# Performance work log

Hardware: AMD Instinct MI355X
Metric: run time of the kernel (lower is better)

The kernel has to match this reference:

```python
import jax, jax.numpy as jnp
import numpy as np
import math

TOPK = 13
NUM_CLASSES = 80
ALPHA = 1.0
BETA = 6.0
EPS = 1e-9


def ciou_xyxy(box1, box2, eps=1e-7):
    """CIoU between xyxy boxes; box1/box2 broadcastable [..., 4]. Returns [..., 1]."""
    b1x1, b1y1, b1x2, b1y2 = jnp.split(box1, 4, axis=-1)
    b2x1, b2y1, b2x2, b2y2 = jnp.split(box2, 4, axis=-1)
    w1, h1 = b1x2 - b1x1, b1y2 - b1y1 + eps
    w2, h2 = b2x2 - b2x1, b2y2 - b2y1 + eps
    inter = (jnp.minimum(b1x2, b2x2) - jnp.maximum(b1x1, b2x1)).clip(0) * \
            (jnp.minimum(b1y2, b2y2) - jnp.maximum(b1y1, b2y1)).clip(0)
    union = w1 * h1 + w2 * h2 - inter + eps
    iou = inter / union
    cw = jnp.maximum(b1x2, b2x2) - jnp.minimum(b1x1, b2x1)
    ch = jnp.maximum(b1y2, b2y2) - jnp.minimum(b1y1, b2y1)
    c2 = cw ** 2 + ch ** 2 + eps
    rho2 = ((b2x1 + b2x2 - b1x1 - b1x2) ** 2 + (b2y1 + b2y2 - b1y1 - b1y2) ** 2) / 4
    v = (4.0 / math.pi ** 2) * (jnp.arctan(w2 / h2) - jnp.arctan(w1 / h1)) ** 2
    alpha = jax.lax.stop_gradient(v / (v - iou + (1 + eps)))  # torch.no_grad block
    return iou - (rho2 / c2 + v * alpha)


def setup_inputs() -> dict:
    key = jax.random.key(0)
    ks = jax.random.split(key, 8)
    bs, M = 16, 64
    # YOLOv8 anchor grid: strides 8/16/32 on a 640x640 image -> 8400 points
    pts = []
    for s, n in ((8, 80), (16, 40), (32, 20)):
        xs = (np.arange(n, dtype=np.float32) + 0.5) * s
        gx, gy = np.meshgrid(xs, xs)
        pts.append(np.stack([gx.ravel(), gy.ravel()], -1))
    anc_points = jnp.asarray(np.concatenate(pts, 0), jnp.float32)  # (8400, 2)
    A = anc_points.shape[0]
    pd_scores = jax.random.uniform(ks[0], (bs, A, NUM_CLASSES), jnp.float32)
    c = jax.random.uniform(ks[1], (bs, A, 2), jnp.float32) * 640.0
    wh = jax.random.uniform(ks[2], (bs, A, 2), jnp.float32) * 120.0 + 8.0
    pd_bboxes = jnp.concatenate([c - wh / 2, c + wh / 2], -1)  # xyxy
    gc = jax.random.uniform(ks[3], (bs, M, 2), jnp.float32) * 560.0 + 40.0
    gwh = jax.random.uniform(ks[4], (bs, M, 2), jnp.float32) * 200.0 + 20.0
    gt_bboxes = jnp.concatenate([gc - gwh / 2, gc + gwh / 2], -1)
    gt_labels = jax.random.randint(ks[5], (bs, M, 1), 0, NUM_CLASSES, dtype=jnp.int32)
    mask_gt = (jax.random.uniform(ks[6], (bs, M, 1)) > 0.25).astype(jnp.float32)
    return {"pd_scores": pd_scores, "pd_bboxes": pd_bboxes, "anc_points": anc_points,
            "gt_labels": gt_labels, "gt_bboxes": gt_bboxes, "mask_gt": mask_gt}


def _assign(pd_scores, pd_bboxes, anc_points, gt_labels, gt_bboxes, mask_gt):
    bs, A, nc = pd_scores.shape
    M = gt_bboxes.shape[1]
    dt = pd_scores.dtype

    # ---- select_candidates_in_gts: anchors inside gt boxes -> (b, M, A) ----
    lt = gt_bboxes[:, :, None, :2]            # (b, M, 1, 2)
    rb = gt_bboxes[:, :, None, 2:]
    xy = anc_points[None, None]               # (1, 1, A, 2)
    deltas = jnp.concatenate([xy - lt, rb - xy], axis=-1)  # (b, M, A, 4)
    mask_in_gts = (deltas.min(-1) > EPS).astype(dt)        # (b, M, A)

    # ---- get_box_metrics ----
    bidx = jnp.arange(bs)[:, None]                         # (b, 1)
    labels = gt_labels[..., 0].astype(jnp.int32)           # (b, M)
    bbox_scores = pd_scores[bidx, :, labels]               # (b, M, A)
    overlaps = ciou_xyxy(gt_bboxes[:, :, None, :], pd_bboxes[:, None, :, :])
    overlaps = overlaps[..., 0].clip(0)                    # (b, M, A)
    align_metric = bbox_scores ** ALPHA * overlaps ** BETA

    # ---- select_topk_candidates (scatter-add instead of one_hot over 8400) ----
    metrics = align_metric * mask_in_gts
    _, topk_idxs = jax.lax.top_k(metrics, TOPK)            # (b, M, topk)
    valid = mask_gt > 0                                    # (b, M, 1) bool
    topk_idxs = jnp.where(valid, topk_idxs, 0)
    counts = jnp.zeros((bs, M, A), dt).at[
        jnp.arange(bs)[:, None, None], jnp.arange(M)[None, :, None], topk_idxs
    ].add(1.0)
    mask_topk = jnp.where(counts > 1, jnp.zeros((), dt), counts)
    mask_pos = mask_topk * mask_in_gts * mask_gt           # (b, M, A)

    # ---- select_highest_overlaps (unconditional; identity when no conflicts) ----
    fg_mask = mask_pos.sum(-2)                             # (b, A)
    mask_multi = fg_mask[:, None, :] > 1                   # (b, 1, A)
    max_idx = overlaps.argmax(1)                           # (b, A)
    is_max = jnp.swapaxes(jax.nn.one_hot(max_idx, M, dtype=dt), 1, 2)  # (b, M, A)
    mask_pos = jnp.where(mask_multi, is_max, mask_pos)
    fg_mask = mask_pos.sum(-2)
    target_gt_idx = mask_pos.argmax(-2)                    # (b, A)

    # ---- get_targets ----
    flat_idx = target_gt_idx + bidx * M                    # (b, A) into b*M
    target_labels = jnp.clip(gt_labels.reshape(-1)[flat_idx], 0)   # (b, A)
    target_bboxes = gt_bboxes.reshape(-1, 4)[flat_idx]             # (b, A, 4)
    target_scores = jax.nn.one_hot(target_labels, NUM_CLASSES, dtype=dt)
    target_scores = jnp.where(fg_mask[..., None] > 0, target_scores, jnp.zeros((), dt))

    # ---- normalize scores by aligned metric ----
    align_metric = align_metric * mask_pos
    pos_align = align_metric.max(-1, keepdims=True)        # (b, M, 1)
    pos_overlaps = (overlaps * mask_pos).max(-1, keepdims=True)
    norm = (align_metric * pos_overlaps / (pos_align + EPS)).max(-2)[..., None]  # (b, A, 1)
    target_scores = target_scores * norm

    return target_labels, target_bboxes, target_scores, fg_mask.astype(bool), target_gt_idx


def reference(pd_scores, pd_bboxes, anc_points, gt_labels, gt_bboxes, mask_gt):
    return _assign(pd_scores, pd_bboxes, anc_points, gt_labels, gt_bboxes, mask_gt)
```

## Files before the change

kernel.cpp:

```cpp
#include <hip/hip_runtime.h>

#define A_TOT 8400
#define NCLS  80
#define MGT   64
#define TK    13
#define NT    256
#define EPS7  1e-7f
#define EPS9  1e-9f
#define INV_PI2 0.4052847345693511f

__device__ __forceinline__ float ciou_clip(
    float gx1, float gy1, float gx2, float gy2, float ga, float area1,
    float px1, float py1, float px2, float py2, float pa)
{
  float w2 = px2 - px1, h2 = py2 - py1 + EPS7;
  float iw = fmaxf(fminf(gx2, px2) - fmaxf(gx1, px1), 0.f);
  float ih = fmaxf(fminf(gy2, py2) - fmaxf(gy1, py1), 0.f);
  float inter = iw * ih;
  float uni = area1 + w2 * h2 - inter + EPS7;
  float iou = inter / uni;
  float cw = fmaxf(gx2, px2) - fminf(gx1, px1);
  float ch = fmaxf(gy2, py2) - fminf(gy1, py1);
  float c2 = cw * cw + ch * ch + EPS7;
  float dx = px1 + px2 - gx1 - gx2;
  float dy = py1 + py2 - gy1 - gy2;
  float rho2 = (dx * dx + dy * dy) * 0.25f;
  float dd = pa - ga;
  float v = INV_PI2 * dd * dd;
  float alpha = v / (v - iou + (1.f + EPS7));
  float c = iou - (rho2 / c2 + v * alpha);
  return fmaxf(c, 0.f);
}

__device__ __forceinline__ unsigned long long wmax64(unsigned long long k) {
#pragma unroll
  for (int s = 32; s > 0; s >>= 1) {
    unsigned long long o = __shfl_xor(k, s, 64);
    k = (o > k) ? o : k;
  }
  return k;
}

__global__ __launch_bounds__(NT)
void k_topk(const float* __restrict__ pd_scores,
            const float* __restrict__ pd_bboxes,
            const float* __restrict__ anc,
            const int* __restrict__ gt_labels,
            const float* __restrict__ gt_bboxes,
            const float* __restrict__ mask_gt,
            unsigned long long* __restrict__ mask64)
{
  int row = blockIdx.x;
  if (mask_gt[row] <= 0.f) return;
  int b = row >> 6;
  int m = row & 63;
  int tid = threadIdx.x, lane = tid & 63, wid = tid >> 6;

  float4 g = ((const float4*)gt_bboxes)[row];
  float ga = atanf((g.z - g.x) / (g.w - g.y + EPS7));
  float area1 = (g.z - g.x) * (g.w - g.y + EPS7);
  int label = gt_labels[row];
  const float*  ps   = pd_scores + (size_t)b * A_TOT * NCLS + label;
  const float4* pb   = (const float4*)(pd_bboxes + (size_t)b * A_TOT * 4);
  const float2* anc2 = (const float2*)anc;

  unsigned long long l[TK];
#pragma unroll
  for (int k = 0; k < TK; ++k) l[k] = 0ULL;

  auto insert = [&](unsigned long long key) {
    if (key > l[TK - 1]) {
#pragma unroll
      for (int j = TK - 1; j > 0; --j) {
        unsigned long long prev = l[j - 1];
        l[j] = (key > prev) ? prev : ((key > l[j]) ? key : l[j]);
      }
      l[0] = (key > l[0]) ? key : l[0];
    }
  };
  auto eval_inbox = [&](int a) -> unsigned long long {
    float4 p = pb[a];
    float pa = atanf((p.z - p.x) / (p.w - p.y + EPS7));
    float ov = ciou_clip(g.x, g.y, g.z, g.w, ga, area1, p.x, p.y, p.z, p.w, pa);
    float o2 = ov * ov;
    float metric = ps[(size_t)a * NCLS] * (o2 * o2 * o2);
    return (((unsigned long long)__float_as_uint(metric)) << 32) |
           (unsigned long long)(~(unsigned)a);
  };

  {
    int a = tid;
    float2 an = anc2[a];
    float dmin = fminf(fminf(an.x - g.x, an.y - g.y), fminf(g.z - an.x, g.w - an.y));
    unsigned long long key = (unsigned long long)(~(unsigned)a);
    if (dmin > EPS9) key = eval_inbox(a);
    insert(key);
  }

  const int   ns[3] = {80, 40, 20};
  const float ss[3] = {8.f, 16.f, 32.f};
  const int   bb[3] = {0, 6400, 8000};
#pragma unroll
  for (int sc = 0; sc < 3; ++sc) {
    int n = ns[sc]; float s = ss[sc]; int base = bb[sc];
    float inv_s = 1.f / s;
    int xlo = max(0,     (int)floorf(g.x * inv_s - 0.5f));
    int xhi = min(n - 1, (int)ceilf (g.z * inv_s - 0.5f));
    int ylo = max(0,     (int)floorf(g.y * inv_s - 0.5f));
    int yhi = min(n - 1, (int)ceilf (g.w * inv_s - 0.5f));
    int nx = xhi - xlo + 1, ny = yhi - ylo + 1;
    if (nx <= 0 || ny <= 0) continue;
    int tot = nx * ny;
    float invnx = 1.f / (float)nx;
    for (int r = tid; r < tot; r += NT) {
      int q  = (int)floorf(((float)r + 0.5f) * invnx);
      int ix = xlo + (r - q * nx);
      int iy = ylo + q;
      int a = base + iy * n + ix;
      if (a < NT) continue;
      float ax = ((float)ix + 0.5f) * s;
      float ay = ((float)iy + 0.5f) * s;
      float dmin = fminf(fminf(ax - g.x, ay - g.y), fminf(g.z - ax, g.w - ay));
      if (dmin > EPS9) insert(eval_inbox(a));
    }
  }

  __shared__ unsigned long long sk[4 * TK];
  unsigned long long wres = 0ULL;
#pragma unroll
  for (int r = 0; r < TK; ++r) {
    unsigned long long w = wmax64(l[0]);
    if (lane == r) wres = w;
    if (l[0] == w) {
#pragma unroll
      for (int j = 0; j < TK - 1; ++j) l[j] = l[j + 1];
      l[TK - 1] = 0ULL;
    }
  }
  if (lane < TK) sk[wid * TK + lane] = wres;
  __syncthreads();

  if (wid == 0) {
    unsigned long long c = (lane < 4 * TK) ? sk[lane] : 0ULL;
    unsigned long long res = 0ULL;
#pragma unroll
    for (int r = 0; r < TK; ++r) {
      unsigned long long w = wmax64(c);
      if (lane == r) res = w;
      if (c == w) c = 0ULL;
    }
    if (lane < TK) {
      unsigned a = ~(unsigned)res;
      float2 an = anc2[a];
      float dmin = fminf(fminf(an.x - g.x, an.y - g.y), fminf(g.z - an.x, g.w - an.y));
      if (dmin > EPS9)
        atomicOr(mask64 + (size_t)b * A_TOT + a, 1ULL << m);
    }
  }
}

__global__ __launch_bounds__(256)
void k_resolve(const float* __restrict__ pd_scores,
               const float* __restrict__ pd_bboxes,
               const int* __restrict__ gt_labels,
               const float* __restrict__ gt_bboxes,
               const unsigned long long* __restrict__ mask64,
               int* __restrict__ tgt_ws, float* __restrict__ am_ws,
               unsigned int* __restrict__ pos_al, unsigned int* __restrict__ pos_ov,
               int total)
{
  int t = blockIdx.x * 256 + threadIdx.x;
  bool valid = t < total;
  unsigned long long msk = valid ? mask64[t] : 0ULL;
  int pc = __popcll(msk);
  float4 p = make_float4(0.f, 0.f, 0.f, 0.f);
  float pa_own = 0.f;
  if (valid && pc >= 1) {
    p = ((const float4*)pd_bboxes)[t];
    pa_own = atanf((p.z - p.x) / (p.w - p.y + EPS7));
  }
  if (valid && pc == 0) tgt_ws[t] = -1;
  if (valid && pc == 1) {
    int b = t / A_TOT;
    int tgt = __ffsll(msk) - 1;
    int gi = b * MGT + tgt;
    float4 g = ((const float4*)gt_bboxes)[gi];
    float ga = atanf((g.z - g.x) / (g.w - g.y + EPS7));
    float area1 = (g.z - g.x) * (g.w - g.y + EPS7);
    float ov = ciou_clip(g.x, g.y, g.z, g.w, ga, area1,
                         p.x, p.y, p.z, p.w, pa_own);
    int label = gt_labels[gi];
    float sc = pd_scores[(size_t)t * NCLS + label];
    float o2 = ov * ov;
    float am = sc * (o2 * o2 * o2);
    tgt_ws[t] = tgt; am_ws[t] = am;
    atomicMax(pos_al + gi, __float_as_uint(am));
    atomicMax(pos_ov + gi, __float_as_uint(ov));
  }
  unsigned long long mb = __ballot(valid && pc > 1);
  int lane = threadIdx.x & 63;
  while (mb) {
    int src = __ffsll(mb) - 1; mb &= mb - 1;
    int   tt  = __shfl(t, src);
    float px1 = __shfl(p.x, src), py1 = __shfl(p.y, src);
    float px2 = __shfl(p.z, src), py2 = __shfl(p.w, src);
    float pa  = __shfl(pa_own, src);
    int bb2 = tt / A_TOT;
    int gi = bb2 * MGT + lane;
    float4 g = ((const float4*)gt_bboxes)[gi];
    float ga = atanf((g.z - g.x) / (g.w - g.y + EPS7));
    float area1 = (g.z - g.x) * (g.w - g.y + EPS7);
    float ov = ciou_clip(g.x, g.y, g.z, g.w, ga, area1,
                         px1, py1, px2, py2, pa);
    unsigned long long key =
        (((unsigned long long)__float_as_uint(ov)) << 6) | (unsigned)(63 - lane);
    unsigned long long w = wmax64(key);
    if (key == w) {
      int label = gt_labels[gi];
      float sc = pd_scores[(size_t)tt * NCLS + label];
      float o2 = ov * ov;
      float am = sc * (o2 * o2 * o2);
      tgt_ws[tt] = lane; am_ws[tt] = am;
      atomicMax(pos_al + gi, __float_as_uint(am));
      atomicMax(pos_ov + gi, __float_as_uint(ov));
    }
  }
}

__global__ __launch_bounds__(256)
void k_write(const int* __restrict__ tgt_ws, const float* __restrict__ am_ws,
             const unsigned int* __restrict__ pos_al,
             const unsigned int* __restrict__ pos_ov,
             const int* __restrict__ gt_labels, const float* __restrict__ gt_bboxes,
             float* __restrict__ out, int bs)
{
  __shared__ int   slab[256];
  __shared__ float snorm[256];
  int total = bs * A_TOT;
  int base = blockIdx.x * 256;
  int t = base + threadIdx.x;
  int nrows = total - base; if (nrows > 256) nrows = 256;
  size_t OFF_BOX = (size_t)total;
  size_t OFF_SCR = OFF_BOX + (size_t)total * 4;
  size_t OFF_FG  = OFF_SCR + (size_t)total * NCLS;
  size_t OFF_TGT = OFF_FG + (size_t)total;
  if (t < total) {
    int b = t / A_TOT;
    int tw = tgt_ws[t];
    bool fg = tw >= 0;
    int tgt = fg ? tw : 0;
    int gi = b * MGT + tgt;
    int lab = gt_labels[gi]; if (lab < 0) lab = 0;
    float4 box = ((const float4*)gt_bboxes)[gi];
    float nrm = 0.f;
    if (fg) {
      float pa_ = __uint_as_float(pos_al[gi]);
      float po  = __uint_as_float(pos_ov[gi]);
      nrm = am_ws[t] * po / (pa_ + EPS9);
    }
    out[t] = (float)lab;
    ((float4*)(out + OFF_BOX))[t] = box;
    out[OFF_FG + t]  = fg ? 1.f : 0.f;
    out[OFF_TGT + t] = (float)tgt;
    slab[threadIdx.x]  = lab;
    snorm[threadIdx.x] = nrm;
  }
  __syncthreads();
  float4* srow = (float4*)(out + OFF_SCR + (size_t)base * NCLS);
  int nvec = nrows * (NCLS / 4);
  for (int u = threadIdx.x; u < nvec; u += 256) {
    int i  = u / (NCLS / 4);
    int c0 = (u - i * (NCLS / 4)) * 4;
    int lb = slab[i]; float nv = snorm[i];
    float4 v;
    v.x = (lb == c0    ) ? nv : 0.f;
    v.y = (lb == c0 + 1) ? nv : 0.f;
    v.z = (lb == c0 + 2) ? nv : 0.f;
    v.w = (lb == c0 + 3) ? nv : 0.f;
    srow[u] = v;
  }
}

extern "C" void kernel_launch(void* const* d_in, const int* in_sizes, int n_in,
                              void* d_out, int out_size, void* d_ws, size_t ws_size,
                              hipStream_t stream)
{
  const float* pd_scores = (const float*)d_in[0];
  const float* pd_bboxes = (const float*)d_in[1];
  const float* anc       = (const float*)d_in[2];
  const int*   gt_labels = (const int*)d_in[3];
  const float* gt_bboxes = (const float*)d_in[4];
  const float* mask_gt   = (const float*)d_in[5];
  int bs = in_sizes[0] / (A_TOT * NCLS);
  int NA = bs * A_TOT, NM = bs * MGT;

  unsigned long long* mask64 = (unsigned long long*)d_ws;
  unsigned int* pos_al = (unsigned int*)(mask64 + NA);
  unsigned int* pos_ov = pos_al + NM;
  int*   tgt_ws = (int*)(pos_ov + NM);
  float* am_ws  = (float*)(tgt_ws + NA);

  hipMemsetAsync(mask64, 0, (size_t)NA * 8 + (size_t)NM * 8, stream);

  k_topk<<<NM, NT, 0, stream>>>(pd_scores, pd_bboxes, anc, gt_labels, gt_bboxes,
                                mask_gt, mask64);
  k_resolve<<<(NA + 255) / 256, 256, 0, stream>>>(pd_scores, pd_bboxes, gt_labels,
                                                  gt_bboxes, mask64,
                                                  tgt_ws, am_ws, pos_al, pos_ov, NA);
  k_write<<<(NA + 255) / 256, 256, 0, stream>>>(tgt_ws, am_ws, pos_al, pos_ov,
                                                gt_labels, gt_bboxes, (float*)d_out, bs);
}
```

Measured before the change: 128.7 us.

## Fuse memset, top-k, resolve and write into one cooperative persistent kernel

Replaces the workspace memset and the three separate kernel launches with one cooperative kernel. It zeroes the workspace itself and separates the phases with grid-wide syncs, looping over rows and tiles with grid-stride loops. The aim is to remove per-launch overhead and the gaps between dependent launches. In exchange it adds three grid barriers and caps the grid at the co-resident block count. It also hardcodes 256 CUs in the grid size and keeps the old multi-kernel path as a fallback if the cooperative launch fails.

```diff
diff --git a/kernel.cpp b/kernel.cpp
--- a/kernel.cpp
+++ b/kernel.cpp
@@ -1,10 +1,12 @@
 #include <hip/hip_runtime.h>
+#include <hip/hip_cooperative_groups.h>
+
+namespace cg = cooperative_groups;
 
 #define A_TOT 8400
 #define NCLS  80
 #define MGT   64
 #define TK    13
-#define NT    256
 #define EPS7  1e-7f
 #define EPS9  1e-9f
 #define INV_PI2 0.4052847345693511f
@@ -41,28 +43,29 @@
   return k;
 }
 
-__global__ __launch_bounds__(NT)
-void k_topk(const float* __restrict__ pd_scores,
-            const float* __restrict__ pd_bboxes,
-            const float* __restrict__ anc,
-            const int* __restrict__ gt_labels,
-            const float* __restrict__ gt_bboxes,
-            const float* __restrict__ mask_gt,
-            unsigned long long* __restrict__ mask64)
-{
-  int row = blockIdx.x;
+
+__device__ __forceinline__ void topk_row_body(
+    int row, int tid,
+    const float* __restrict__ pd_scores,
+    const float* __restrict__ pd_bboxes,
+    const float2* __restrict__ anc2,
+    const int* __restrict__ gt_labels,
+    const float4* __restrict__ gb,
+    const float* __restrict__ mask_gt,
+    unsigned long long* __restrict__ mask64,
+    unsigned long long* sk)
+{
   if (mask_gt[row] <= 0.f) return;
   int b = row >> 6;
   int m = row & 63;
-  int tid = threadIdx.x, lane = tid & 63, wid = tid >> 6;
-
-  float4 g = ((const float4*)gt_bboxes)[row];
+  int lane = tid & 63, wid = tid >> 6;
+
+  float4 g = gb[row];
   float ga = atanf((g.z - g.x) / (g.w - g.y + EPS7));
   float area1 = (g.z - g.x) * (g.w - g.y + EPS7);
   int label = gt_labels[row];
-  const float*  ps   = pd_scores + (size_t)b * A_TOT * NCLS + label;
-  const float4* pb   = (const float4*)(pd_bboxes + (size_t)b * A_TOT * 4);
-  const float2* anc2 = (const float2*)anc;
+  const float*  ps = pd_scores + (size_t)b * A_TOT * NCLS + label;
+  const float4* pb = (const float4*)(pd_bboxes + (size_t)b * A_TOT * 4);
 
   unsigned long long l[TK];
 #pragma unroll
@@ -112,12 +115,12 @@
     if (nx <= 0 || ny <= 0) continue;
     int tot = nx * ny;
     float invnx = 1.f / (float)nx;
-    for (int r = tid; r < tot; r += NT) {
+    for (int r = tid; r < tot; r += 256) {
       int q  = (int)floorf(((float)r + 0.5f) * invnx);
       int ix = xlo + (r - q * nx);
       int iy = ylo + q;
       int a = base + iy * n + ix;
-      if (a < NT) continue;
+      if (a < 256) continue;
       float ax = ((float)ix + 0.5f) * s;
       float ay = ((float)iy + 0.5f) * s;
       float dmin = fminf(fminf(ax - g.x, ay - g.y), fminf(g.z - ax, g.w - ay));
@@ -125,7 +128,6 @@
     }
   }
 
-  __shared__ unsigned long long sk[4 * TK];
   unsigned long long wres = 0ULL;
 #pragma unroll
   for (int r = 0; r < TK; ++r) {
@@ -159,18 +161,17 @@
   }
 }
 
-__global__ __launch_bounds__(256)
-void k_resolve(const float* __restrict__ pd_scores,
-               const float* __restrict__ pd_bboxes,
-               const int* __restrict__ gt_labels,
-               const float* __restrict__ gt_bboxes,
-               const unsigned long long* __restrict__ mask64,
-               int* __restrict__ tgt_ws, float* __restrict__ am_ws,
-               unsigned int* __restrict__ pos_al, unsigned int* __restrict__ pos_ov,
-               int total)
-{
-  int t = blockIdx.x * 256 + threadIdx.x;
-  bool valid = t < total;
+__device__ __forceinline__ void resolve_body(
+    int t, bool valid,
+    const float* __restrict__ pd_scores,
+    const float* __restrict__ pd_bboxes,
+    const int* __restrict__ gt_labels,
+    const float4* __restrict__ gb,
+    const unsigned long long* __restrict__ mask64,
+    int* __restrict__ tgt_ws, float* __restrict__ am_ws,
+    unsigned int* __restrict__ pos_al, unsigned int* __restrict__ pos_ov)
+{
+  int lane = threadIdx.x & 63;
   unsigned long long msk = valid ? mask64[t] : 0ULL;
   int pc = __popcll(msk);
   float4 p = make_float4(0.f, 0.f, 0.f, 0.f);
@@ -184,7 +185,7 @@
     int b = t / A_TOT;
     int tgt = __ffsll(msk) - 1;
     int gi = b * MGT + tgt;
-    float4 g = ((const float4*)gt_bboxes)[gi];
+    float4 g = gb[gi];
     float ga = atanf((g.z - g.x) / (g.w - g.y + EPS7));
     float area1 = (g.z - g.x) * (g.w - g.y + EPS7);
     float ov = ciou_clip(g.x, g.y, g.z, g.w, ga, area1,
@@ -198,7 +199,6 @@
     atomicMax(pos_ov + gi, __float_as_uint(ov));
   }
   unsigned long long mb = __ballot(valid && pc > 1);
-  int lane = threadIdx.x & 63;
   while (mb) {
     int src = __ffsll(mb) - 1; mb &= mb - 1;
     int   tt  = __shfl(t, src);
@@ -207,7 +207,7 @@
     float pa  = __shfl(pa_own, src);
     int bb2 = tt / A_TOT;
     int gi = bb2 * MGT + lane;
-    float4 g = ((const float4*)gt_bboxes)[gi];
+    float4 g = gb[gi];
     float ga = atanf((g.z - g.x) / (g.w - g.y + EPS7));
     float area1 = (g.z - g.x) * (g.w - g.y + EPS7);
     float ov = ciou_clip(g.x, g.y, g.z, g.w, ga, area1,
@@ -227,32 +227,29 @@
   }
 }
 
-__global__ __launch_bounds__(256)
-void k_write(const int* __restrict__ tgt_ws, const float* __restrict__ am_ws,
-             const unsigned int* __restrict__ pos_al,
-             const unsigned int* __restrict__ pos_ov,
-             const int* __restrict__ gt_labels, const float* __restrict__ gt_bboxes,
-             float* __restrict__ out, int bs)
-{
-  __shared__ int   slab[256];
-  __shared__ float snorm[256];
-  int total = bs * A_TOT;
-  int base = blockIdx.x * 256;
-  int t = base + threadIdx.x;
+__device__ __forceinline__ void write_body(
+    int base, int tid, int total,
+    const int* __restrict__ tgt_ws, const float* __restrict__ am_ws,
+    const unsigned int* __restrict__ pos_al,
+    const unsigned int* __restrict__ pos_ov,
+    const int* __restrict__ gt_labels, const float4* __restrict__ gb,
+    float* __restrict__ out, int* slab, float* snorm)
+{
+  int t = base + tid;
   int nrows = total - base; if (nrows > 256) nrows = 256;
   size_t OFF_BOX = (size_t)total;
   size_t OFF_SCR = OFF_BOX + (size_t)total * 4;
   size_t OFF_FG  = OFF_SCR + (size_t)total * NCLS;
   size_t OFF_TGT = OFF_FG + (size_t)total;
+  int lab = 0; float nrm = 0.f;
   if (t < total) {
     int b = t / A_TOT;
     int tw = tgt_ws[t];
     bool fg = tw >= 0;
     int tgt = fg ? tw : 0;
     int gi = b * MGT + tgt;
-    int lab = gt_labels[gi]; if (lab < 0) lab = 0;
-    float4 box = ((const float4*)gt_bboxes)[gi];
-    float nrm = 0.f;
+    lab = gt_labels[gi]; if (lab < 0) lab = 0;
+    float4 box = gb[gi];
     if (fg) {
       float pa_ = __uint_as_float(pos_al[gi]);
       float po  = __uint_as_float(pos_ov[gi]);
@@ -262,13 +259,13 @@
     ((float4*)(out + OFF_BOX))[t] = box;
     out[OFF_FG + t]  = fg ? 1.f : 0.f;
     out[OFF_TGT + t] = (float)tgt;
-    slab[threadIdx.x]  = lab;
-    snorm[threadIdx.x] = nrm;
-  }
+  }
+  slab[tid]  = lab;
+  snorm[tid] = nrm;
   __syncthreads();
   float4* srow = (float4*)(out + OFF_SCR + (size_t)base * NCLS);
   int nvec = nrows * (NCLS / 4);
-  for (int u = threadIdx.x; u < nvec; u += 256) {
+  for (int u = tid; u < nvec; u += 256) {
     int i  = u / (NCLS / 4);
     int c0 = (u - i * (NCLS / 4)) * 4;
     int lb = slab[i]; float nv = snorm[i];
@@ -281,6 +278,102 @@
   }
 }
 
+__global__ __launch_bounds__(256)
+void k_fused(const float* __restrict__ pd_scores,
+             const float* __restrict__ pd_bboxes,
+             const float* __restrict__ anc,
+             const int* __restrict__ gt_labels,
+             const float* __restrict__ gt_bboxes,
+             const float* __restrict__ mask_gt,
+             unsigned long long* __restrict__ mask64,
+             unsigned int* __restrict__ pos_al,
+             unsigned int* __restrict__ pos_ov,
+             int* __restrict__ tgt_ws, float* __restrict__ am_ws,
+             float* __restrict__ out, int bs)
+{
+  cg::grid_group grid = cg::this_grid();
+  const int NA = bs * A_TOT, NM = bs * MGT;
+  const int gsize = gridDim.x * 256;
+  const int gtid = blockIdx.x * 256 + threadIdx.x;
+  const int tid = threadIdx.x;
+
+  __shared__ unsigned long long sk[4 * TK];
+  __shared__ int   slab[256];
+  __shared__ float snorm[256];
+
+  const float2* anc2 = (const float2*)anc;
+  const float4* gb   = (const float4*)gt_bboxes;
+
+  for (int i = gtid; i < NA; i += gsize) mask64[i] = 0ULL;
+  for (int i = gtid; i < 2 * NM; i += gsize) pos_al[i] = 0u;
+  grid.sync();
+
+  for (int row = blockIdx.x; row < NM; row += gridDim.x) {
+    topk_row_body(row, tid, pd_scores, pd_bboxes, anc2, gt_labels, gb,
+                  mask_gt, mask64, sk);
+    __syncthreads();
+  }
+  grid.sync();
+
+  for (int t0 = 0; t0 < NA; t0 += gsize) {
+    int t = t0 + gtid;
+    resolve_body(t, t < NA, pd_scores, pd_bboxes, gt_labels, gb, mask64,
+                 tgt_ws, am_ws, pos_al, pos_ov);
+  }
+  grid.sync();
+
+  int ntiles = (NA + 255) >> 8;
+  for (int tile = blockIdx.x; tile < ntiles; tile += gridDim.x) {
+    write_body(tile << 8, tid, NA, tgt_ws, am_ws, pos_al, pos_ov,
+               gt_labels, gb, out, slab, snorm);
+    __syncthreads();
+  }
+}
+
+__global__ __launch_bounds__(256)
+void k_topk_sa(const float* __restrict__ pd_scores,
+               const float* __restrict__ pd_bboxes,
+               const float* __restrict__ anc,
+               const int* __restrict__ gt_labels,
+               const float* __restrict__ gt_bboxes,
+               const float* __restrict__ mask_gt,
+               unsigned long long* __restrict__ mask64)
+{
+  __shared__ unsigned long long sk[4 * TK];
+  topk_row_body(blockIdx.x, threadIdx.x, pd_scores, pd_bboxes,
+                (const float2*)anc, gt_labels, (const float4*)gt_bboxes,
+                mask_gt, mask64, sk);
+}
+
+__global__ __launch_bounds__(256)
+void k_resolve_sa(const float* __restrict__ pd_scores,
+                  const float* __restrict__ pd_bboxes,
+                  const int* __restrict__ gt_labels,
+                  const float* __restrict__ gt_bboxes,
+                  const unsigned long long* __restrict__ mask64,
+                  int* __restrict__ tgt_ws, float* __restrict__ am_ws,
+                  unsigned int* __restrict__ pos_al,
+                  unsigned int* __restrict__ pos_ov, int total)
+{
+  int t = blockIdx.x * 256 + threadIdx.x;
+  resolve_body(t, t < total, pd_scores, pd_bboxes, gt_labels,
+               (const float4*)gt_bboxes, mask64, tgt_ws, am_ws, pos_al, pos_ov);
+}
+
+__global__ __launch_bounds__(256)
+void k_write_sa(const int* __restrict__ tgt_ws, const float* __restrict__ am_ws,
+                const unsigned int* __restrict__ pos_al,
+                const unsigned int* __restrict__ pos_ov,
+                const int* __restrict__ gt_labels,
+                const float* __restrict__ gt_bboxes,
+                float* __restrict__ out, int total)
+{
+  __shared__ int   slab[256];
+  __shared__ float snorm[256];
+  write_body(blockIdx.x * 256, threadIdx.x, total, tgt_ws, am_ws, pos_al,
+             pos_ov, gt_labels, (const float4*)gt_bboxes, out, slab, snorm);
+}
+
 extern "C" void kernel_launch(void* const* d_in, const int* in_sizes, int n_in,
                               void* d_out, int out_size, void* d_ws, size_t ws_size,
                               hipStream_t stream)
@@ -299,14 +392,35 @@
   unsigned int* pos_ov = pos_al + NM;
   int*   tgt_ws = (int*)(pos_ov + NM);
   float* am_ws  = (float*)(tgt_ws + NA);
-
-  hipMemsetAsync(mask64, 0, (size_t)NA * 8 + (size_t)NM * 8, stream);
-
-  k_topk<<<NM, NT, 0, stream>>>(pd_scores, pd_bboxes, anc, gt_labels, gt_bboxes,
-                                mask_gt, mask64);
-  k_resolve<<<(NA + 255) / 256, 256, 0, stream>>>(pd_scores, pd_bboxes, gt_labels,
-                                                  gt_bboxes, mask64,
-                                                  tgt_ws, am_ws, pos_al, pos_ov, NA);
-  k_write<<<(NA + 255) / 256, 256, 0, stream>>>(tgt_ws, am_ws, pos_al, pos_ov,
-                                                gt_labels, gt_bboxes, (float*)d_out, bs);
-}
+  float* out = (float*)d_out;
+
+  hipError_t lerr = hipErrorUnknown;
+  int blocksPerCU = 0;
+  hipError_t qerr = hipOccupancyMaxActiveBlocksPerMultiprocessor(
+      &blocksPerCU, k_fused, 256, 0);
+  if (qerr == hipSuccess && blocksPerCU > 0) {
+    int G = blocksPerCU * 256;
+    int need = (NA + 255) / 256; if (need < NM) need = NM;
+    if (G > need) G = need;
+    void* args[] = {
+      (void*)&pd_scores, (void*)&pd_bboxes, (void*)&anc, (void*)&gt_labels,
+      (void*)&gt_bboxes, (void*)&mask_gt, (void*)&mask64, (void*)&pos_al,
+      (void*)&pos_ov, (void*)&tgt_ws, (void*)&am_ws, (void*)&out, (void*)&bs
+    };
+    lerr = hipLaunchCooperativeKernel((void*)k_fused, dim3(G), dim3(256),
+                                      args, 0, stream);
+  }
+
+  if (lerr != hipSuccess) {
+    hipMemsetAsync(mask64, 0, (size_t)NA * 8 + (size_t)NM * 8, stream);
+    k_topk_sa<<<NM, 256, 0, stream>>>(pd_scores, pd_bboxes, anc, gt_labels,
+                                      gt_bboxes, mask_gt, mask64);
+    k_resolve_sa<<<(NA + 255) / 256, 256, 0, stream>>>(pd_scores, pd_bboxes,
+                                                       gt_labels, gt_bboxes,
+                                                       mask64, tgt_ws, am_ws,
+                                                       pos_al, pos_ov, NA);
+    k_write_sa<<<(NA + 255) / 256, 256, 0, stream>>>(tgt_ws, am_ws, pos_al,
+                                                     pos_ov, gt_labels,
+                                                     gt_bboxes, out, NA);
+  }
+}
```

After: 282.0 us. 2.19x slower.

## Replace global bitmask atomics with per-batch shared-memory resolve and packed outputs

Applied to the files above, without the earlier changes.

The top-k kernel now writes its 13 selected anchor indices per ground truth, instead of atomically OR-ing bits into a global 64-bit mask that had to be memset first. A new resolve kernel runs one 1024-thread block per image. It counts assignments in shared memory, resolves multi-assigned anchors by a wave argmax over CIoU, and keeps the per-GT max reductions in shared atomics. It then writes a packed 64-bit record of target, label, foreground flag and normalisation for the final writer. This removes the memset, the global atomics and the intermediate workspace traffic, but resolution now runs on only batch-size blocks, which leaves most of the GPU idle during that stage.

```diff
diff --git a/kernel.cpp b/kernel.cpp
--- a/kernel.cpp
+++ b/kernel.cpp
@@ -4,10 +4,11 @@
 #define NCLS  80
 #define MGT   64
 #define TK    13
-#define NT    256
 #define EPS7  1e-7f
 #define EPS9  1e-9f
 #define INV_PI2 0.4052847345693511f
+#define BTH   1024
+#define NIT   ((A_TOT + BTH - 1) / BTH)
 
 __device__ __forceinline__ float ciou_clip(
     float gx1, float gy1, float gx2, float gy2, float ga, float area1,
@@ -41,20 +42,24 @@
   return k;
 }
 
-__global__ __launch_bounds__(NT)
-void k_topk(const float* __restrict__ pd_scores,
-            const float* __restrict__ pd_bboxes,
-            const float* __restrict__ anc,
-            const int* __restrict__ gt_labels,
-            const float* __restrict__ gt_bboxes,
-            const float* __restrict__ mask_gt,
-            unsigned long long* __restrict__ mask64)
+__global__ __launch_bounds__(256)
+void k_topkA(const float* __restrict__ pd_scores,
+             const float* __restrict__ pd_bboxes,
+             const float* __restrict__ anc,
+             const int* __restrict__ gt_labels,
+             const float* __restrict__ gt_bboxes,
+             const float* __restrict__ mask_gt,
+             int* __restrict__ topk_idx)
 {
   int row = blockIdx.x;
-  if (mask_gt[row] <= 0.f) return;
+  int tid = threadIdx.x, lane = tid & 63, wid = tid >> 6;
+  __shared__ unsigned long long sk[4 * TK];
+
+  if (mask_gt[row] <= 0.f) {
+    if (tid < TK) topk_idx[row * TK + tid] = -1;
+    return;
+  }
   int b = row >> 6;
-  int m = row & 63;
-  int tid = threadIdx.x, lane = tid & 63, wid = tid >> 6;
 
   float4 g = ((const float4*)gt_bboxes)[row];
   float ga = atanf((g.z - g.x) / (g.w - g.y + EPS7));
@@ -112,12 +117,12 @@
     if (nx <= 0 || ny <= 0) continue;
     int tot = nx * ny;
     float invnx = 1.f / (float)nx;
-    for (int r = tid; r < tot; r += NT) {
+    for (int r = tid; r < tot; r += 256) {
       int q  = (int)floorf(((float)r + 0.5f) * invnx);
       int ix = xlo + (r - q * nx);
       int iy = ylo + q;
       int a = base + iy * n + ix;
-      if (a < NT) continue;
+      if (a < 256) continue;
       float ax = ((float)ix + 0.5f) * s;
       float ay = ((float)iy + 0.5f) * s;
       float dmin = fminf(fminf(ax - g.x, ay - g.y), fminf(g.z - ax, g.w - ay));
@@ -125,7 +130,6 @@
     }
   }
 
-  __shared__ unsigned long long sk[4 * TK];
   unsigned long long wres = 0ULL;
 #pragma unroll
   for (int r = 0; r < TK; ++r) {
@@ -153,122 +157,158 @@
       unsigned a = ~(unsigned)res;
       float2 an = anc2[a];
       float dmin = fminf(fminf(an.x - g.x, an.y - g.y), fminf(g.z - an.x, g.w - an.y));
-      if (dmin > EPS9)
-        atomicOr(mask64 + (size_t)b * A_TOT + a, 1ULL << m);
-    }
+      topk_idx[row * TK + lane] = (dmin > EPS9) ? (int)a : -1;
+    }
+  }
+}
+
+__global__ __launch_bounds__(BTH)
+void k_resolveB(const float* __restrict__ pd_scores,
+                const float* __restrict__ pd_bboxes,
+                const int* __restrict__ gt_labels,
+                const float* __restrict__ gt_bboxes,
+                const int* __restrict__ topk_idx,
+                unsigned long long* __restrict__ pk)
+{
+  int b = blockIdx.x;
+  int tid = threadIdx.x, lane = tid & 63;
+  __shared__ unsigned int cntm[A_TOT];
+  __shared__ float4 sg[MGT];
+  __shared__ float  sga[MGT], sarea[MGT];
+  __shared__ int    slabm[MGT];
+  __shared__ unsigned int spal[MGT], spov[MGT];
+
+  for (int i = tid; i < A_TOT; i += BTH) cntm[i] = 0u;
+  if (tid < MGT) {
+    float4 g = ((const float4*)gt_bboxes)[b * MGT + tid];
+    sg[tid] = g;
+    sga[tid] = atanf((g.z - g.x) / (g.w - g.y + EPS7));
+    sarea[tid] = (g.z - g.x) * (g.w - g.y + EPS7);
+    slabm[tid] = gt_labels[b * MGT + tid];
+    spal[tid] = 0u; spov[tid] = 0u;
+  }
+  __syncthreads();
+
+  if (tid < MGT * TK) {
+    int a = topk_idx[b * MGT * TK + tid];
+    if (a >= 0) atomicAdd(&cntm[a], (1u << 16) | (unsigned)(tid / TK));
+  }
+  __syncthreads();
+
+  const float4* pb = (const float4*)pd_bboxes + (size_t)b * A_TOT;
+  const float*  ps = pd_scores + (size_t)b * A_TOT * NCLS;
+
+  int   rtgt[NIT];
+  float ram[NIT];
+
+#pragma unroll
+  for (int it = 0; it < NIT; ++it) {
+    int a = tid + it * BTH;
+    bool valid = a < A_TOT;
+    unsigned cm = valid ? cntm[a] : 0u;
+    int cnt = (int)(cm >> 16);
+    float4 p = make_float4(0.f, 0.f, 0.f, 0.f);
+    float pa = 0.f;
+    if (valid && cnt > 0) {
+      p = pb[a];
+      pa = atanf((p.z - p.x) / (p.w - p.y + EPS7));
+    }
+    int mytgt = -1; float myam = 0.f;
+    if (valid && cnt == 1) {
+      int m = (int)(cm & 0xffffu);
+      float4 g = sg[m];
+      float ov = ciou_clip(g.x, g.y, g.z, g.w, sga[m], sarea[m],
+                           p.x, p.y, p.z, p.w, pa);
+      float o2 = ov * ov;
+      myam = ps[(size_t)a * NCLS + slabm[m]] * (o2 * o2 * o2);
+      mytgt = m;
+      atomicMax(&spal[m], __float_as_uint(myam));
+      atomicMax(&spov[m], __float_as_uint(ov));
+    }
+    unsigned long long mb = __ballot(valid && cnt > 1);
+    while (mb) {
+      int src = __ffsll(mb) - 1; mb &= mb - 1;
+      int   aa  = __shfl(a, src);
+      float px1 = __shfl(p.x, src), py1 = __shfl(p.y, src);
+      float px2 = __shfl(p.z, src), py2 = __shfl(p.w, src);
+      float spa = __shfl(pa, src);
+      float4 g = sg[lane];
+      float ov = ciou_clip(g.x, g.y, g.z, g.w, sga[lane], sarea[lane],
+                           px1, py1, px2, py2, spa);
+      unsigned long long key =
+          (((unsigned long long)__float_as_uint(ov)) << 6) | (unsigned)(63 - lane);
+      unsigned long long w = wmax64(key);
+      int   wl  = 63 - (int)(w & 63ULL);
+      float wov = __uint_as_float((unsigned)(w >> 6));
+      float am_s = 0.f;
+      if (lane == wl) {
+        float o2 = wov * wov;
+        am_s = ps[(size_t)aa * NCLS + slabm[wl]] * (o2 * o2 * o2);
+        atomicMax(&spal[wl], __float_as_uint(am_s));
+        atomicMax(&spov[wl], __float_as_uint(wov));
+      }
+      am_s = __shfl(am_s, wl);
+      if (lane == src) { mytgt = wl; myam = am_s; }
+    }
+    rtgt[it] = mytgt; ram[it] = myam;
+  }
+  __syncthreads();
+
+#pragma unroll
+  for (int it = 0; it < NIT; ++it) {
+    int a = tid + it * BTH;
+    if (a >= A_TOT) continue;
+    int mytgt = rtgt[it];
+    bool fg = mytgt >= 0;
+    int tgt = fg ? mytgt : 0;
+    int lab = slabm[tgt]; if (lab < 0) lab = 0;
+    float nrm = 0.f;
+    if (fg) {
+      float pal = __uint_as_float(spal[tgt]);
+      float pov = __uint_as_float(spov[tgt]);
+      nrm = ram[it] * pov / (pal + EPS9);
+    }
+    unsigned lo = (unsigned)tgt | ((unsigned)lab << 8) | ((fg ? 1u : 0u) << 24);
+    pk[(size_t)b * A_TOT + a] =
+        (((unsigned long long)__float_as_uint(nrm)) << 32) | lo;
   }
 }
 
 __global__ __launch_bounds__(256)
-void k_resolve(const float* __restrict__ pd_scores,
-               const float* __restrict__ pd_bboxes,
-               const int* __restrict__ gt_labels,
-               const float* __restrict__ gt_bboxes,
-               const unsigned long long* __restrict__ mask64,
-               int* __restrict__ tgt_ws, float* __restrict__ am_ws,
-               unsigned int* __restrict__ pos_al, unsigned int* __restrict__ pos_ov,
-               int total)
-{
-  int t = blockIdx.x * 256 + threadIdx.x;
-  bool valid = t < total;
-  unsigned long long msk = valid ? mask64[t] : 0ULL;
-  int pc = __popcll(msk);
-  float4 p = make_float4(0.f, 0.f, 0.f, 0.f);
-  float pa_own = 0.f;
-  if (valid && pc >= 1) {
-    p = ((const float4*)pd_bboxes)[t];
-    pa_own = atanf((p.z - p.x) / (p.w - p.y + EPS7));
-  }
-  if (valid && pc == 0) tgt_ws[t] = -1;
-  if (valid && pc == 1) {
-    int b = t / A_TOT;
-    int tgt = __ffsll(msk) - 1;
-    int gi = b * MGT + tgt;
-    float4 g = ((const float4*)gt_bboxes)[gi];
-    float ga = atanf((g.z - g.x) / (g.w - g.y + EPS7));
-    float area1 = (g.z - g.x) * (g.w - g.y + EPS7);
-    float ov = ciou_clip(g.x, g.y, g.z, g.w, ga, area1,
-                         p.x, p.y, p.z, p.w, pa_own);
-    int label = gt_labels[gi];
-    float sc = pd_scores[(size_t)t * NCLS + label];
-    float o2 = ov * ov;
-    float am = sc * (o2 * o2 * o2);
-    tgt_ws[t] = tgt; am_ws[t] = am;
-    atomicMax(pos_al + gi, __float_as_uint(am));
-    atomicMax(pos_ov + gi, __float_as_uint(ov));
-  }
-  unsigned long long mb = __ballot(valid && pc > 1);
-  int lane = threadIdx.x & 63;
-  while (mb) {
-    int src = __ffsll(mb) - 1; mb &= mb - 1;
-    int   tt  = __shfl(t, src);
-    float px1 = __shfl(p.x, src), py1 = __shfl(p.y, src);
-    float px2 = __shfl(p.z, src), py2 = __shfl(p.w, src);
-    float pa  = __shfl(pa_own, src);
-    int bb2 = tt / A_TOT;
-    int gi = bb2 * MGT + lane;
-    float4 g = ((const float4*)gt_bboxes)[gi];
-    float ga = atanf((g.z - g.x) / (g.w - g.y + EPS7));
-    float area1 = (g.z - g.x) * (g.w - g.y + EPS7);
-    float ov = ciou_clip(g.x, g.y, g.z, g.w, ga, area1,
-                         px1, py1, px2, py2, pa);
-    unsigned long long key =
-        (((unsigned long long)__float_as_uint(ov)) << 6) | (unsigned)(63 - lane);
-    unsigned long long w = wmax64(key);
-    if (key == w) {
-      int label = gt_labels[gi];
-      float sc = pd_scores[(size_t)tt * NCLS + label];
-      float o2 = ov * ov;
-      float am = sc * (o2 * o2 * o2);
-      tgt_ws[tt] = lane; am_ws[tt] = am;
-      atomicMax(pos_al + gi, __float_as_uint(am));
-      atomicMax(pos_ov + gi, __float_as_uint(ov));
-    }
-  }
-}
-
-__global__ __launch_bounds__(256)
-void k_write(const int* __restrict__ tgt_ws, const float* __restrict__ am_ws,
-             const unsigned int* __restrict__ pos_al,
-             const unsigned int* __restrict__ pos_ov,
-             const int* __restrict__ gt_labels, const float* __restrict__ gt_bboxes,
-             float* __restrict__ out, int bs)
+void k_writeC(const unsigned long long* __restrict__ pk,
+              const float* __restrict__ gt_bboxes,
+              float* __restrict__ out, int total)
 {
   __shared__ int   slab[256];
   __shared__ float snorm[256];
-  int total = bs * A_TOT;
-  int base = blockIdx.x * 256;
-  int t = base + threadIdx.x;
+  int base = blockIdx.x * 256, tid = threadIdx.x;
+  int t = base + tid;
   int nrows = total - base; if (nrows > 256) nrows = 256;
   size_t OFF_BOX = (size_t)total;
   size_t OFF_SCR = OFF_BOX + (size_t)total * 4;
   size_t OFF_FG  = OFF_SCR + (size_t)total * NCLS;
   size_t OFF_TGT = OFF_FG + (size_t)total;
+  int lab = 0; float nrm = 0.f;
   if (t < total) {
+    unsigned long long v = pk[t];
+    unsigned lo = (unsigned)v;
+    int tgt = (int)(lo & 0xffu);
+    lab = (int)((lo >> 8) & 0xffu);
+    bool fg = (lo >> 24) & 1u;
+    nrm = __uint_as_float((unsigned)(v >> 32));
     int b = t / A_TOT;
-    int tw = tgt_ws[t];
-    bool fg = tw >= 0;
-    int tgt = fg ? tw : 0;
-    int gi = b * MGT + tgt;
-    int lab = gt_labels[gi]; if (lab < 0) lab = 0;
-    float4 box = ((const float4*)gt_bboxes)[gi];
-    float nrm = 0.f;
-    if (fg) {
-      float pa_ = __uint_as_float(pos_al[gi]);
-      float po  = __uint_as_float(pos_ov[gi]);
-      nrm = am_ws[t] * po / (pa_ + EPS9);
-    }
+    float4 box = ((const float4*)gt_bboxes)[b * MGT + tgt];
     out[t] = (float)lab;
     ((float4*)(out + OFF_BOX))[t] = box;
     out[OFF_FG + t]  = fg ? 1.f : 0.f;
     out[OFF_TGT + t] = (float)tgt;
-    slab[threadIdx.x]  = lab;
-    snorm[threadIdx.x] = nrm;
-  }
+  }
+  slab[tid]  = lab;
+  snorm[tid] = nrm;
   __syncthreads();
   float4* srow = (float4*)(out + OFF_SCR + (size_t)base * NCLS);
   int nvec = nrows * (NCLS / 4);
-  for (int u = threadIdx.x; u < nvec; u += 256) {
+  for (int u = tid; u < nvec; u += 256) {
     int i  = u / (NCLS / 4);
     int c0 = (u - i * (NCLS / 4)) * 4;
     int lb = slab[i]; float nv = snorm[i];
@@ -294,19 +334,13 @@
   int bs = in_sizes[0] / (A_TOT * NCLS);
   int NA = bs * A_TOT, NM = bs * MGT;
 
-  unsigned long long* mask64 = (unsigned long long*)d_ws;
-  unsigned int* pos_al = (unsigned int*)(mask64 + NA);
-  unsigned int* pos_ov = pos_al + NM;
-  int*   tgt_ws = (int*)(pos_ov + NM);
-  float* am_ws  = (float*)(tgt_ws + NA);
-
-  hipMemsetAsync(mask64, 0, (size_t)NA * 8 + (size_t)NM * 8, stream);
-
-  k_topk<<<NM, NT, 0, stream>>>(pd_scores, pd_bboxes, anc, gt_labels, gt_bboxes,
-                                mask_gt, mask64);
-  k_resolve<<<(NA + 255) / 256, 256, 0, stream>>>(pd_scores, pd_bboxes, gt_labels,
-                                                  gt_bboxes, mask64,
-                                                  tgt_ws, am_ws, pos_al, pos_ov, NA);
-  k_write<<<(NA + 255) / 256, 256, 0, stream>>>(tgt_ws, am_ws, pos_al, pos_ov,
-                                                gt_labels, gt_bboxes, (float*)d_out, bs);
-}
+  unsigned long long* pk = (unsigned long long*)d_ws;
+  int* topk_idx = (int*)(pk + NA);
+
+  k_topkA<<<NM, 256, 0, stream>>>(pd_scores, pd_bboxes, anc, gt_labels,
+                                  gt_bboxes, mask_gt, topk_idx);
+  k_resolveB<<<bs, BTH, 0, stream>>>(pd_scores, pd_bboxes, gt_labels,
+                                     gt_bboxes, topk_idx, pk);
+  k_writeC<<<(NA + 255) / 256, 256, 0, stream>>>(pk, gt_bboxes,
+                                                 (float*)d_out, NA);
+}
```

New measurement: 137.4 us. 1.07x slower.
